# Kernel optimization log

Measured on AMD Instinct MI355X. Metric: run time of the kernel, lower is better.

## Reference

```python
import jax, jax.numpy as jnp
import numpy as np

B, S, H = 4, 2048, 1024
NH, HD = 16, 64  # num heads, head dim
SCALE = 1.0 / np.sqrt(HD).astype(np.float32)
CLAMP = 1e9
EPS = 1e-9

def setup_inputs() -> dict:
    key = jax.random.key(0)
    ks = jax.random.split(key, 4)
    w_std = 0.02
    return {
        "hidden_states": jax.random.normal(ks[0], (B, S, H), dtype=jnp.float32),
        "Wq": jax.random.normal(ks[1], (H, H), dtype=jnp.float32) * w_std,
        "bq": jnp.zeros((H,), dtype=jnp.float32),
        "Wk": jax.random.normal(ks[2], (H, H), dtype=jnp.float32) * w_std,
        "bk": jnp.zeros((H,), dtype=jnp.float32),
        "Wv": jax.random.normal(ks[3], (H, H), dtype=jnp.float32) * w_std,
        "bv": jnp.zeros((H,), dtype=jnp.float32),
    }

def reference(hidden_states, Wq, bq, Wk, bk, Wv, bv):
    b, s, h = hidden_states.shape
    # linear projections, then split heads: [B,S,H] -> [B,S,NH,HD]
    q = (hidden_states @ Wq + bq).reshape(b, s, NH, HD)
    k = (hidden_states @ Wk + bk).reshape(b, s, NH, HD)
    v = (hidden_states @ Wv + bv).reshape(b, s, NH, HD)
    # scores: [B,NH,Sq,Sk]
    scores = jnp.einsum("bqhd,bkhd->bhqk", q, k) * SCALE
    scores = jnp.clip(scores, -CLAMP, CLAMP)
    probs = jax.nn.softmax(scores, axis=-1) + EPS
    # dropout: eval mode (identity)
    ctx = jnp.einsum("bhqk,bkhd->bqhd", probs, v)
    return ctx.reshape(b, s, h)
```

## Files before the change

### kernel.cpp

```cpp
#include <hip/hip_runtime.h>
#include <hip/hip_bf16.h>
#include <stdint.h>

#define B_ 4
#define S_ 2048
#define H_ 1024
#define NH_ 16
#define HD_ 64
#define SCALE_ 0.125f
#define LOG2E_ 1.4426950408889634f

typedef __bf16 bf16x8 __attribute__((ext_vector_type(8)));
typedef float f32x4 __attribute__((ext_vector_type(4)));
typedef unsigned short us4 __attribute__((ext_vector_type(4)));
typedef unsigned short us8 __attribute__((ext_vector_type(8)));
typedef unsigned short ushort_t;

__device__ __forceinline__ ushort_t f2bf(float f) {
  union { float f; uint32_t u; } a; a.f = f;
  uint32_t r = (a.u + 0x7fffu + ((a.u >> 16) & 1u)) >> 16;
  return (ushort_t)r;
}

__device__ __forceinline__ void async16(const void* g, void* l) {
  __builtin_amdgcn_global_load_lds(
      (const __attribute__((address_space(1))) unsigned int*)(uintptr_t)g,
      (__attribute__((address_space(3))) unsigned int*)(uintptr_t)l, 16, 0, 0);
}

__global__ __launch_bounds__(256) void conv_x(const float4* __restrict__ x,
                                              ushort_t* __restrict__ xb) {
  int i = blockIdx.x * 256 + threadIdx.x;
  float4 v = x[i];
  us4 o;
  o.x = f2bf(v.x); o.y = f2bf(v.y); o.z = f2bf(v.z); o.w = f2bf(v.w);
  *(us4*)(xb + (size_t)i * 4) = o;
}

__global__ __launch_bounds__(256) void conv_w(const float* __restrict__ Wq,
                                              const float* __restrict__ Wk,
                                              const float* __restrict__ Wv,
                                              ushort_t* __restrict__ Wt) {
  __shared__ __align__(16) ushort_t T[64 * 64];
  int bid = blockIdx.x;
  int w = bid >> 8;
  int t2 = bid & 255;
  int kt = (t2 >> 4) * 64, nt = (t2 & 15) * 64;
  const float* W = (w == 0) ? Wq : (w == 1) ? Wk : Wv;
  int tid = threadIdx.x;
  int k = tid >> 2, nq = tid & 3;
#pragma unroll
  for (int j4 = 0; j4 < 4; ++j4) {
    int n = nq * 4 + j4 * 16;
    float4 f = *(const float4*)(W + (size_t)(kt + k) * H_ + nt + n);
    us4 o;
    o.x = f2bf(f.x); o.y = f2bf(f.y); o.z = f2bf(f.z); o.w = f2bf(f.w);
    *(us4*)(T + k * 64 + (((n >> 3) ^ (k & 7)) * 8) + (n & 7)) = o;
  }
  __syncthreads();
  int n2 = tid >> 2, kq = tid & 3;
  us8 o0, o1;
#pragma unroll
  for (int j = 0; j < 16; ++j) {
    int kk = kq * 16 + j;
    ushort_t v = T[kk * 64 + (((n2 >> 3) ^ (kk & 7)) * 8) + (n2 & 7)];
    if (j < 8) o0[j] = v; else o1[j - 8] = v;
  }
  size_t obase = (size_t)w * (H_ * H_) + (size_t)(nt + n2) * H_ + kt + kq * 16;
  *(us8*)(Wt + obase) = o0;
  *(us8*)(Wt + obase + 8) = o1;
}

__global__ __launch_bounds__(256) void qkv_gemm(const ushort_t* __restrict__ Xb,
                                                const ushort_t* __restrict__ Wt,
                                                const float* __restrict__ bq,
                                                const float* __restrict__ bk,
                                                const float* __restrict__ bv,
                                                ushort_t* __restrict__ QKV) {
  __shared__ __align__(16) ushort_t As[128 * 32];
  __shared__ __align__(16) ushort_t Bs[128 * 32];
  int nb = blockIdx.x;
  int mb = blockIdx.y;
  int w = nb >> 3;
  int n_base = (nb & 7) * 128;
  int m_base = mb * 128;
  const ushort_t* Wtw = Wt + (size_t)w * (H_ * H_);
  int tid = threadIdx.x;
  int lane = tid & 63, wave = tid >> 6;
  int wr = wave >> 1, wc = wave & 1;
  int g = lane >> 4, l15 = lane & 15;

  f32x4 acc[4][4];
#pragma unroll
  for (int i = 0; i < 4; i++)
#pragma unroll
    for (int j = 0; j < 4; j++) acc[i][j] = (f32x4){0.f, 0.f, 0.f, 0.f};

  for (int kt = 0; kt < 32; ++kt) {
    int k0 = kt * 32;
    __syncthreads();
#pragma unroll
    for (int it = 0; it < 2; ++it) {
      int chunk = tid + it * 256;
      int r = chunk >> 2, c = chunk & 3;
      async16(Xb + (size_t)(m_base + r) * H_ + k0 + c * 8, As + chunk * 8);
      async16(Wtw + (size_t)(n_base + r) * H_ + k0 + c * 8, Bs + chunk * 8);
    }
    __builtin_amdgcn_s_waitcnt(0);
    __syncthreads();

    bf16x8 af[4], bf[4];
#pragma unroll
    for (int mi = 0; mi < 4; mi++)
      af[mi] = *(const bf16x8*)(As + (wr * 64 + mi * 16 + l15) * 32 + g * 8);
#pragma unroll
    for (int ni = 0; ni < 4; ni++)
      bf[ni] = *(const bf16x8*)(Bs + (wc * 64 + ni * 16 + l15) * 32 + g * 8);
#pragma unroll
    for (int mi = 0; mi < 4; mi++)
#pragma unroll
      for (int ni = 0; ni < 4; ni++)
        acc[mi][ni] = __builtin_amdgcn_mfma_f32_16x16x32_bf16(af[mi], bf[ni], acc[mi][ni], 0, 0, 0);
  }

  const float* bias = (w == 0) ? bq : (w == 1) ? bk : bv;
  float mult = (w == 0) ? SCALE_ * LOG2E_ : 1.0f;
  if (w == 2) {
    ushort_t* Vout = QKV + 16777216u;
#pragma unroll
    for (int ni = 0; ni < 4; ++ni) {
      int n_col = n_base + wc * 64 + ni * 16 + l15;
      float bb = bias[n_col];
      int hh = n_col >> 6, d = n_col & 63;
#pragma unroll
      for (int mi = 0; mi < 4; ++mi) {
        int m_row = m_base + wr * 64 + mi * 16 + g * 4;
        int bbi = m_row >> 11, s = m_row & 2047;
        us4 o;
#pragma unroll
        for (int reg = 0; reg < 4; ++reg) o[reg] = f2bf(acc[mi][ni][reg] + bb);
        *(us4*)(Vout + ((size_t)((bbi * 16 + hh) * 64 + d)) * 2048 + s) = o;
      }
    }
  } else {
    ushort_t* out = QKV + (size_t)w * (8192u * 1024u);
#pragma unroll
    for (int ni = 0; ni < 4; ++ni) {
      int n_col = n_base + wc * 64 + ni * 16 + l15;
      float bb = bias[n_col];
#pragma unroll
      for (int mi = 0; mi < 4; ++mi) {
        int m_row = m_base + wr * 64 + mi * 16 + g * 4;
#pragma unroll
        for (int reg = 0; reg < 4; ++reg) {
          float v = (acc[mi][ni][reg] + bb) * mult;
          out[(size_t)(m_row + reg) * H_ + n_col] = f2bf(v);
        }
      }
    }
  }
}

__global__ __launch_bounds__(256, 2) void attn(const ushort_t* __restrict__ QKV,
                                               const ushort_t* __restrict__ Vt,
                                               float* __restrict__ out) {
  __shared__ __align__(16) ushort_t Ks[2][64 * 64];
  __shared__ __align__(16) ushort_t Vs[2][64 * 64];
  int qt = blockIdx.x;
  int bh = blockIdx.y;
  int b = bh >> 4, h = bh & 15;
  int tid = threadIdx.x, lane = tid & 63, wave = tid >> 6;
  int g = lane >> 4, l15 = lane & 15;

  const ushort_t* Qb = QKV;
  const ushort_t* Kb = QKV + 8388608u;

  bf16x8 qf[4][2];
#pragma unroll
  for (int mi = 0; mi < 4; ++mi) {
    int q_row = qt * 256 + wave * 64 + mi * 16 + l15;
    size_t qoff = (size_t)(b * S_ + q_row) * H_ + h * HD_;
    qf[mi][0] = *(const bf16x8*)(Qb + qoff + g * 8);
    qf[mi][1] = *(const bf16x8*)(Qb + qoff + 32 + g * 8);
  }

  union { us8 u; bf16x8 v; } ones_u;
#pragma unroll
  for (int i = 0; i < 8; ++i) ones_u.u[i] = 0x3F80;
  bf16x8 onesf = ones_u.v;

  f32x4 of[4][4];
  f32x4 lacc[4];
#pragma unroll
  for (int mi = 0; mi < 4; mi++) {
    lacc[mi] = (f32x4){0.f, 0.f, 0.f, 0.f};
#pragma unroll
    for (int ni = 0; ni < 4; ni++) of[mi][ni] = (f32x4){0.f, 0.f, 0.f, 0.f};
  }

  int ra = (l15 >> 2) * 8 + (l15 & 3);
  int sKa = ((l15 >> 2) & 1) * 4 + (l15 & 3);
  int posK0 = (g ^ sKa) * 8, posK1 = ((4 + g) ^ sKa) * 8;

  int ch0 = tid, ch1 = tid + 256;
  int s0 = ch0 >> 3, s1 = ch1 >> 3;
  int cK0 = (ch0 & 7) ^ ((((s0 >> 3) & 1) << 2) | (s0 & 3));
  int cK1 = (ch1 & 7) ^ ((((s1 >> 3) & 1) << 2) | (s1 & 3));
  int cV0 = (ch0 & 7) ^ (s0 & 7);
  int cV1 = (ch1 & 7) ^ (s1 & 7);
  const ushort_t* srcK0 = Kb + (size_t)(b * S_ + s0) * H_ + h * HD_ + cK0 * 8;
  const ushort_t* srcK1 = Kb + (size_t)(b * S_ + s1) * H_ + h * HD_ + cK1 * 8;
  const ushort_t* srcV0 = Vt + ((size_t)bh * 64 + s0) * S_ + cV0 * 8;
  const ushort_t* srcV1 = Vt + ((size_t)bh * 64 + s1) * S_ + cV1 * 8;

  async16(srcK0, Ks[0] + ch0 * 8);
  async16(srcK1, Ks[0] + ch1 * 8);
  async16(srcV0, Vs[0] + ch0 * 8);
  async16(srcV1, Vs[0] + ch1 * 8);

  for (int kb = 0; kb < 32; ++kb) {
    int cur = kb & 1, nxt = cur ^ 1;
    __syncthreads();
    if (kb < 31) {
      async16(srcK0 + (size_t)(kb + 1) * 64 * H_, Ks[nxt] + ch0 * 8);
      async16(srcK1 + (size_t)(kb + 1) * 64 * H_, Ks[nxt] + ch1 * 8);
      async16(srcV0 + (size_t)(kb + 1) * 64, Vs[nxt] + ch0 * 8);
      async16(srcV1 + (size_t)(kb + 1) * 64, Vs[nxt] + ch1 * 8);
      __builtin_amdgcn_s_waitcnt(0xF74);
    } else {
      __builtin_amdgcn_s_waitcnt(0xF70);
    }
    __syncthreads();
    const ushort_t* Kc = Ks[cur];
    const ushort_t* Vc = Vs[cur];

#pragma unroll
    for (int kk = 0; kk < 2; ++kk) {
      int rowa = kk * 32 + ra;
      int rowb = rowa + 4;
      bf16x8 ka0 = *(const bf16x8*)(Kc + rowa * 64 + posK0);
      bf16x8 ka1 = *(const bf16x8*)(Kc + rowa * 64 + posK1);
      bf16x8 kb0 = *(const bf16x8*)(Kc + rowb * 64 + posK0);
      bf16x8 kb1 = *(const bf16x8*)(Kc + rowb * 64 + posK1);
      bf16x8 vf[4];
#pragma unroll
      for (int ni = 0; ni < 4; ++ni) {
        int row = ni * 16 + l15;
        vf[ni] = *(const bf16x8*)(Vc + row * 64 + (((kk * 4 + g) ^ (row & 7)) * 8));
      }
#pragma unroll
      for (int mi = 0; mi < 4; ++mi) {
        f32x4 sa = (f32x4){0.f, 0.f, 0.f, 0.f};
        f32x4 sb = (f32x4){0.f, 0.f, 0.f, 0.f};
        sa = __builtin_amdgcn_mfma_f32_16x16x32_bf16(ka0, qf[mi][0], sa, 0, 0, 0);
        sa = __builtin_amdgcn_mfma_f32_16x16x32_bf16(ka1, qf[mi][1], sa, 0, 0, 0);
        sb = __builtin_amdgcn_mfma_f32_16x16x32_bf16(kb0, qf[mi][0], sb, 0, 0, 0);
        sb = __builtin_amdgcn_mfma_f32_16x16x32_bf16(kb1, qf[mi][1], sb, 0, 0, 0);
        float pa0 = __builtin_amdgcn_exp2f(sa[0]);
        float pa1 = __builtin_amdgcn_exp2f(sa[1]);
        float pa2 = __builtin_amdgcn_exp2f(sa[2]);
        float pa3 = __builtin_amdgcn_exp2f(sa[3]);
        float pb0 = __builtin_amdgcn_exp2f(sb[0]);
        float pb1 = __builtin_amdgcn_exp2f(sb[1]);
        float pb2 = __builtin_amdgcn_exp2f(sb[2]);
        float pb3 = __builtin_amdgcn_exp2f(sb[3]);
        union { bf16x8 v; unsigned int u[4]; } pf;
        pf.u[0] = __builtin_amdgcn_perm(__float_as_uint(pa1) + 0x8000u,
                                        __float_as_uint(pa0) + 0x8000u, 0x07060302u);
        pf.u[1] = __builtin_amdgcn_perm(__float_as_uint(pa3) + 0x8000u,
                                        __float_as_uint(pa2) + 0x8000u, 0x07060302u);
        pf.u[2] = __builtin_amdgcn_perm(__float_as_uint(pb1) + 0x8000u,
                                        __float_as_uint(pb0) + 0x8000u, 0x07060302u);
        pf.u[3] = __builtin_amdgcn_perm(__float_as_uint(pb3) + 0x8000u,
                                        __float_as_uint(pb2) + 0x8000u, 0x07060302u);
#pragma unroll
        for (int ni = 0; ni < 4; ++ni)
          of[mi][ni] = __builtin_amdgcn_mfma_f32_16x16x32_bf16(vf[ni], pf.v, of[mi][ni], 0, 0, 0);
        lacc[mi] = __builtin_amdgcn_mfma_f32_16x16x32_bf16(onesf, pf.v, lacc[mi], 0, 0, 0);
      }
    }
  }

#pragma unroll
  for (int mi = 0; mi < 4; ++mi) {
    float inv = 1.0f / lacc[mi][0];
    int qglob = qt * 256 + wave * 64 + mi * 16 + l15;
    float* obase = out + (size_t)(b * S_ + qglob) * H_ + h * HD_ + g * 4;
#pragma unroll
    for (int ni = 0; ni < 4; ++ni) {
      float4 vv;
      vv.x = of[mi][ni][0] * inv;
      vv.y = of[mi][ni][1] * inv;
      vv.z = of[mi][ni][2] * inv;
      vv.w = of[mi][ni][3] * inv;
      *(float4*)(obase + ni * 16) = vv;
    }
  }
}

extern "C" void kernel_launch(void* const* d_in, const int* in_sizes, int n_in,
                              void* d_out, int out_size, void* d_ws, size_t ws_size,
                              hipStream_t stream) {
  const float* hs = (const float*)d_in[0];
  const float* Wq = (const float*)d_in[1];
  const float* bq = (const float*)d_in[2];
  const float* Wk = (const float*)d_in[3];
  const float* bk = (const float*)d_in[4];
  const float* Wv = (const float*)d_in[5];
  const float* bv = (const float*)d_in[6];
  float* out = (float*)d_out;

  ushort_t* Xb  = (ushort_t*)d_ws;
  ushort_t* Wt  = Xb + 8388608u;
  ushort_t* QKV = Wt + 3145728u;
  ushort_t* Vtp = QKV + 16777216u;

  conv_x<<<8192, 256, 0, stream>>>((const float4*)hs, Xb);
  conv_w<<<768, 256, 0, stream>>>(Wq, Wk, Wv, Wt);
  qkv_gemm<<<dim3(24, 64), 256, 0, stream>>>(Xb, Wt, bq, bk, bv, QKV);
  attn<<<dim3(8, 64), 256, 0, stream>>>(QKV, Vtp, out);
}
```

Measured before the change: 245.3 us.

## Double-buffer QKV GEMM shared tiles and swizzle block order

Splits the QKV projection GEMM's shared-memory A/B tiles into two buffers so the async global loads for the next K-step are issued before the MFMAs on the current step, using a partial vmcnt wait instead of draining all loads. It also remaps block indices so consecutive blocks are spread across M rows, which changes L2 reuse of weight and activation tiles. The cost is double the LDS per block, which may reduce occupancy, plus reliance on hand-encoded waitcnt values being correct.

```diff
diff --git a/kernel.cpp b/kernel.cpp
--- a/kernel.cpp
+++ b/kernel.cpp
@@ -77,10 +77,12 @@
                                                 const float* __restrict__ bk,
                                                 const float* __restrict__ bv,
                                                 ushort_t* __restrict__ QKV) {
-  __shared__ __align__(16) ushort_t As[128 * 32];
-  __shared__ __align__(16) ushort_t Bs[128 * 32];
-  int nb = blockIdx.x;
-  int mb = blockIdx.y;
+  __shared__ __align__(16) ushort_t As[2][128 * 32];
+  __shared__ __align__(16) ushort_t Bs[2][128 * 32];
+  int flat = blockIdx.y * 24 + blockIdx.x;
+  int nf = (flat & 7) * 192 + (flat >> 3);
+  int mb = nf / 24;
+  int nb = nf - mb * 24;
   int w = nb >> 3;
   int n_base = (nb & 7) * 128;
   int m_base = mb * 128;
@@ -96,26 +98,40 @@
 #pragma unroll
     for (int j = 0; j < 4; j++) acc[i][j] = (f32x4){0.f, 0.f, 0.f, 0.f};
 
+  int r0 = tid >> 2, c = tid & 3;
+  const ushort_t* sA0 = Xb + (size_t)(m_base + r0) * H_ + c * 8;
+  const ushort_t* sA1 = sA0 + (size_t)64 * H_;
+  const ushort_t* sB0 = Wtw + (size_t)(n_base + r0) * H_ + c * 8;
+  const ushort_t* sB1 = sB0 + (size_t)64 * H_;
+  int la0 = tid * 8, la1 = (tid + 256) * 8;
+
+  async16(sA0, As[0] + la0);
+  async16(sA1, As[0] + la1);
+  async16(sB0, Bs[0] + la0);
+  async16(sB1, Bs[0] + la1);
+
   for (int kt = 0; kt < 32; ++kt) {
-    int k0 = kt * 32;
+    int cur = kt & 1, nxt = cur ^ 1;
     __syncthreads();
-#pragma unroll
-    for (int it = 0; it < 2; ++it) {
-      int chunk = tid + it * 256;
-      int r = chunk >> 2, c = chunk & 3;
-      async16(Xb + (size_t)(m_base + r) * H_ + k0 + c * 8, As + chunk * 8);
-      async16(Wtw + (size_t)(n_base + r) * H_ + k0 + c * 8, Bs + chunk * 8);
-    }
-    __builtin_amdgcn_s_waitcnt(0);
+    if (kt < 31) {
+      int k0 = (kt + 1) * 32;
+      async16(sA0 + k0, As[nxt] + la0);
+      async16(sA1 + k0, As[nxt] + la1);
+      async16(sB0 + k0, Bs[nxt] + la0);
+      async16(sB1 + k0, Bs[nxt] + la1);
+      __builtin_amdgcn_s_waitcnt(0xF74);
+    } else {
+      __builtin_amdgcn_s_waitcnt(0xF70);
+    }
     __syncthreads();
 
     bf16x8 af[4], bf[4];
 #pragma unroll
     for (int mi = 0; mi < 4; mi++)
-      af[mi] = *(const bf16x8*)(As + (wr * 64 + mi * 16 + l15) * 32 + g * 8);
+      af[mi] = *(const bf16x8*)(As[cur] + (wr * 64 + mi * 16 + l15) * 32 + g * 8);
 #pragma unroll
     for (int ni = 0; ni < 4; ni++)
-      bf[ni] = *(const bf16x8*)(Bs + (wc * 64 + ni * 16 + l15) * 32 + g * 8);
+      bf[ni] = *(const bf16x8*)(Bs[cur] + (wc * 64 + ni * 16 + l15) * 32 + g * 8);
 #pragma unroll
     for (int mi = 0; mi < 4; mi++)
 #pragma unroll
```

New measurement: 256.9 us. 4.7% more time.
